# Optimization experiments

Measured on AMD Instinct MI355X. Metric: run time of the kernel, lower is better.

Reference implementation:

```python
import jax, jax.numpy as jnp
import numpy as np

D_MODEL = 1024
N_HEAD = 16
D_HEAD = D_MODEL // N_HEAD
FFN_HIDDEN = 4096
NEG_INF = -1e30


def sinusoid_pos_emb(pos_seq, d_model):
    # pos_seq: [K] descending relative positions; returns [K, d_model]
    inv_freq = 1.0 / (10000.0 ** (jnp.arange(0, d_model, 2, dtype=jnp.float32) / d_model))
    ang = pos_seq[:, None] * inv_freq[None, :]
    return jnp.concatenate([jnp.sin(ang), jnp.cos(ang)], axis=-1)


def rel_shift(x):
    # x: [B, H, Q, K] -> Transformer-XL relative shift
    b, h, q, k = x.shape
    x = jnp.pad(x, ((0, 0), (0, 0), (0, 0), (1, 0)))
    x = x.reshape(b, h, k + 1, q)[:, :, 1:, :].reshape(b, h, q, k)
    return x


def layer_norm(x, g, b, eps=1e-5):
    mu = jnp.mean(x, axis=-1, keepdims=True)
    var = jnp.var(x, axis=-1, keepdims=True)
    return (x - mu) * jax.lax.rsqrt(var + eps) * g + b


def setup_inputs() -> dict:
    key = jax.random.key(0)
    ks = jax.random.split(key, 20)
    B, T, M = 4, 2048, 2048
    s = 0.02
    inp = {
        "x": jax.random.normal(ks[0], (B, T, D_MODEL), jnp.float32),
        "mem": jax.random.normal(ks[1], (B, M, D_MODEL), jnp.float32),
        "Wq": jax.random.normal(ks[2], (D_MODEL, D_MODEL), jnp.float32) * s,
        "bq": jnp.zeros((D_MODEL,), jnp.float32),
        "Wk": jax.random.normal(ks[3], (D_MODEL, D_MODEL), jnp.float32) * s,
        "bk": jnp.zeros((D_MODEL,), jnp.float32),
        "Wv": jax.random.normal(ks[4], (D_MODEL, D_MODEL), jnp.float32) * s,
        "bv": jnp.zeros((D_MODEL,), jnp.float32),
        "Wo": jax.random.normal(ks[5], (D_MODEL, D_MODEL), jnp.float32) * s,
        "bo": jnp.zeros((D_MODEL,), jnp.float32),
        "Wr": jax.random.normal(ks[6], (D_MODEL, D_MODEL), jnp.float32) * s,
        "u": jax.random.normal(ks[7], (N_HEAD, D_HEAD), jnp.float32) * s,
        "v": jax.random.normal(ks[8], (N_HEAD, D_HEAD), jnp.float32) * s,
        "g1": jnp.ones((D_MODEL,), jnp.float32),
        "be1": jnp.zeros((D_MODEL,), jnp.float32),
        "g2": jnp.ones((D_MODEL,), jnp.float32),
        "be2": jnp.zeros((D_MODEL,), jnp.float32),
        "W1": jax.random.normal(ks[9], (D_MODEL, FFN_HIDDEN), jnp.float32) * s,
        "b1": jnp.zeros((FFN_HIDDEN,), jnp.float32),
        "W2": jax.random.normal(ks[10], (FFN_HIDDEN, D_MODEL), jnp.float32) * s,
        "b2": jnp.zeros((D_MODEL,), jnp.float32),
        "is_causal": 1,
    }
    return inp


def xl_attention(x, mem, Wq, bq, Wk, bk, Wv, bv, Wo, bo, Wr, u, v, is_causal):
    B, T, D = x.shape
    M = mem.shape[1]
    K = M + T
    c = jnp.concatenate([mem, x], axis=1)  # [B, K, D]
    q = (x @ Wq + bq).reshape(B, T, N_HEAD, D_HEAD)
    k = (c @ Wk + bk).reshape(B, K, N_HEAD, D_HEAD)
    vv = (c @ Wv + bv).reshape(B, K, N_HEAD, D_HEAD)
    pos_seq = jnp.arange(K - 1, -1, -1, dtype=jnp.float32)
    r = (sinusoid_pos_emb(pos_seq, D) @ Wr).reshape(K, N_HEAD, D_HEAD)
    # content term + relative-position term (Transformer-XL eq. A+C and B+D)
    AC = jnp.einsum('bihd,bjhd->bhij', q + u, k)
    BD = rel_shift(jnp.einsum('bihd,jhd->bhij', q + v, r))
    score = (AC + BD) * (1.0 / np.sqrt(D_HEAD))
    if is_causal:
        i = jnp.arange(T)[:, None]
        j = jnp.arange(K)[None, :]
        causal = (j <= i + M)  # query i may attend keys up to its own position
        score = jnp.where(causal[None, None], score, NEG_INF)
    attn = jax.nn.softmax(score, axis=-1)
    out = jnp.einsum('bhij,bjhd->bihd', attn, vv).reshape(B, T, D)
    return out @ Wo + bo


def reference(x, mem, Wq, bq, Wk, bk, Wv, bv, Wo, bo, Wr, u, v,
              g1, be1, g2, be2, W1, b1, W2, b2, is_causal):
    # dropout is identity at inference
    a = xl_attention(x, mem, Wq, bq, Wk, bk, Wv, bv, Wo, bo, Wr, u, v, is_causal)
    h = layer_norm(a + x, g1, be1)
    f = jax.nn.gelu(h @ W1 + b1) @ W2 + b2
    return layer_norm(f + h, g2, be2)
```

## Files before the change

### kernel.cpp

```cpp
#include <hip/hip_runtime.h>
#include <stdint.h>

typedef unsigned short u16;
typedef short s16x8 __attribute__((ext_vector_type(8)));
typedef unsigned short u16x4 __attribute__((ext_vector_type(4)));
typedef float f32x4 __attribute__((ext_vector_type(4)));

#define DEV static __device__ __forceinline__

DEV u16 f2b(float f) {
  union { float f; unsigned u; } v; v.f = f;
  unsigned r = v.u + 0x7fffu + ((v.u >> 16) & 1u);
  return (u16)(r >> 16);
}
DEV float b2f(u16 b) {
  union { unsigned u; float f; } v; v.u = ((unsigned)b) << 16; return v.f;
}
DEV unsigned pk_trunc(float a, float b) {
  return __builtin_amdgcn_perm(__float_as_uint(b), __float_as_uint(a), 0x07060302u);
}
DEV f32x4 MFMA16(s16x8 a, s16x8 b, f32x4 c) {
  return __builtin_amdgcn_mfma_f32_16x16x32_bf16(a, b, c, 0, 0, 0);
}
#define GLD_LDS16(gp, lp)                                                            \
  __builtin_amdgcn_global_load_lds((const __attribute__((address_space(1))) void*)(gp), \
                                   (__attribute__((address_space(3))) void*)(lp), 16, 0, 0)


__global__ __launch_bounds__(256) void wt_cast_t(const float* __restrict__ W,
                                                 u16* __restrict__ Wt, int Kd, int Nd) {
  __shared__ float tile[32][33];
  const int n0 = blockIdx.x * 32, k0 = blockIdx.y * 32;
  const int t = threadIdx.x;
#pragma unroll
  for (int p = 0; p < 4; ++p) {
    int idx = p * 256 + t; int r = idx >> 5, c = idx & 31;
    tile[r][c] = W[(long)(k0 + r) * Nd + n0 + c];
  }
  __syncthreads();
#pragma unroll
  for (int p = 0; p < 4; ++p) {
    int idx = p * 256 + t; int r = idx >> 5, c = idx & 31;
    Wt[(long)(n0 + r) * Kd + k0 + c] = f2b(tile[c][r]);
  }
}

__global__ __launch_bounds__(256) void build_cb(const float* __restrict__ x,
                                                const float* __restrict__ mem,
                                                u16* __restrict__ cb) {
  long idx = (long)blockIdx.x * 256 + threadIdx.x;
  long e4 = idx * 4;
  int b = (int)(e4 >> 22);
  long rem = e4 & ((1L << 22) - 1);
  int tok = (int)(rem >> 10);
  int d = (int)(rem & 1023);
  const float* src = (tok < 2048) ? &mem[((long)b * 2048 + tok) * 1024 + d]
                                  : &x[((long)b * 2048 + (tok - 2048)) * 1024 + d];
  float4 vv = *(const float4*)src;
  uint2 o;
  o.x = (unsigned)f2b(vv.x) | ((unsigned)f2b(vv.y) << 16);
  o.y = (unsigned)f2b(vv.z) | ((unsigned)f2b(vv.w) << 16);
  *(uint2*)&cb[e4] = o;
}

__global__ __launch_bounds__(256) void pos_emb(u16* __restrict__ pe) {
  const int d = blockIdx.x;
  const int e0 = threadIdx.x * 4;
  u16 o[4];
#pragma unroll
  for (int i = 0; i < 4; ++i) {
    int e = e0 + i;
    int f = (e < 512) ? e : (e - 512);
    float invf = expf(-(float)f * (9.210340371976184f / 512.f));
    float ang = (float)d * invf;
    o[i] = f2b((e < 512) ? sinf(ang) : cosf(ang));
  }
  uint2 pk; pk.x = (unsigned)o[0] | ((unsigned)o[1] << 16);
  pk.y = (unsigned)o[2] | ((unsigned)o[3] << 16);
  *(uint2*)&pe[(long)d * 1024 + e0] = pk;
}

#define EPI_BF16 0
#define EPI_F32 1
#define EPI_GELU 2
#define EPI_VT 3

template <int EPI, int QMAP>
__global__ __launch_bounds__(256) void gemm_bt(const u16* __restrict__ A,
                                               const u16* __restrict__ Bt,
                                               const float* __restrict__ bias,
                                               void* __restrict__ outp, int Ndim, int Kdim) {
  __shared__ __align__(16) u16 As[128 * 64];
  __shared__ __align__(16) u16 Bs[128 * 64];
  const int col0 = blockIdx.x * 128;
  const int row0 = blockIdx.y * 128;
  const int t = threadIdx.x;
  const int w = t >> 6, l = t & 63;
  const int wr = (w >> 1) * 64, wc = (w & 1) * 64;
  const int lr = l & 15, g = l >> 4;
  f32x4 acc[4][4];
#pragma unroll
  for (int m = 0; m < 4; ++m)
#pragma unroll
    for (int n = 0; n < 4; ++n) acc[m][n] = f32x4{0.f, 0.f, 0.f, 0.f};

  for (int k0 = 0; k0 < Kdim; k0 += 64) {
#pragma unroll
    for (int it = 0; it < 4; ++it) {
      int c = it * 256 + t;
      int r = c >> 3, ch = (c & 7) ^ (r & 7);
      long ga = row0 + r;
      if (QMAP) ga = ((ga >> 11) << 12) + 2048 + (ga & 2047);
      GLD_LDS16(A + ga * Kdim + k0 + ch * 8, &As[c * 8]);
      GLD_LDS16(Bt + (long)(col0 + r) * Kdim + k0 + ch * 8, &Bs[c * 8]);
    }
    __syncthreads();
#pragma unroll
    for (int kk = 0; kk < 2; ++kk) {
      s16x8 af[4], bfv[4];
#pragma unroll
      for (int m = 0; m < 4; ++m) {
        int rm = wr + m * 16 + lr;
        af[m] = *(const s16x8*)&As[rm * 64 + (((g + 4 * kk) ^ (rm & 7)) << 3)];
      }
#pragma unroll
      for (int n = 0; n < 4; ++n) {
        int rn = wc + n * 16 + lr;
        bfv[n] = *(const s16x8*)&Bs[rn * 64 + (((g + 4 * kk) ^ (rn & 7)) << 3)];
      }
#pragma unroll
      for (int m = 0; m < 4; ++m)
#pragma unroll
        for (int n = 0; n < 4; ++n) acc[m][n] = MFMA16(af[m], bfv[n], acc[m][n]);
    }
    __syncthreads();
  }

  const int lg = g * 4;
#pragma unroll
  for (int m = 0; m < 4; ++m) {
    int rbase = row0 + wr + m * 16 + lg;
#pragma unroll
    for (int n = 0; n < 4; ++n) {
      int gc = col0 + wc + n * 16 + lr;
      float bv = bias ? bias[gc] : 0.f;
#pragma unroll
      for (int rg = 0; rg < 4; ++rg) {
        float vv = acc[m][n][rg] + bv;
        ((u16*)outp)[(long)(rbase + rg) * Ndim + gc] = f2b(vv);
      }
    }
  }
}

template <int EPI, int QMAP, int BN>
__global__ __launch_bounds__(512) void gemm_big(const u16* __restrict__ A,
                                                const u16* __restrict__ Bt,
                                                const float* __restrict__ bias,
                                                void* __restrict__ outp, int Ndim, int Kdim) {
  constexpr int NF = BN / 64;
  __shared__ __align__(16) u16 As[2][256 * 64];
  __shared__ __align__(16) u16 Bs[2][BN * 64];
  const int col0 = blockIdx.x * BN;
  const int row0 = blockIdx.y * 256;
  const int t = threadIdx.x;
  const int w = t >> 6, l = t & 63;
  const int wr = (w >> 2) * 128, wc = (w & 3) * (BN / 4);
  const int lr = l & 15, g = l >> 4;

  f32x4 acc[8][NF];
#pragma unroll
  for (int m = 0; m < 8; ++m)
#pragma unroll
    for (int n = 0; n < NF; ++n) acc[m][n] = f32x4{0.f, 0.f, 0.f, 0.f};

  auto stageA = [&](int k0, int p, int nb) {
    int c = p * 512 + t;
    int r = c >> 3, ch = (c & 7) ^ (r & 7);
    long ga = row0 + r;
    if (QMAP) ga = ((ga >> 11) << 12) + 2048 + (ga & 2047);
    GLD_LDS16(A + ga * Kdim + k0 + ch * 8, &As[nb][c * 8]);
  };
  auto stageB = [&](int k0, int p, int nb) {
    int c = p * 512 + t;
    int r = c >> 3, ch = (c & 7) ^ (r & 7);
    GLD_LDS16(Bt + (long)(col0 + r) * Kdim + k0 + ch * 8, &Bs[nb][c * 8]);
  };

  const int nt = Kdim >> 6;
#pragma unroll
  for (int p = 0; p < 4; ++p) stageA(0, p, 0);
#pragma unroll
  for (int p = 0; p < NF; ++p) stageB(0, p, 0);
  __syncthreads();
  int cur = 0;

  for (int ti = 0; ti < nt; ++ti) {
    const int k1 = (ti + 1) << 6;
    const int nb = cur ^ 1;
    s16x8 bf[NF][2];
#pragma unroll
    for (int p = 0; p < 4; ++p) {
      s16x8 af[2][2];
#pragma unroll
      for (int i = 0; i < 2; ++i) {
        int rm = wr + (2 * p + i) * 16 + lr;
#pragma unroll
        for (int kk = 0; kk < 2; ++kk)
          af[i][kk] = *(const s16x8*)&As[cur][rm * 64 + (((g + 4 * kk) ^ (rm & 7)) << 3)];
      }
      if (p == 0) {
#pragma unroll
        for (int n = 0; n < NF; ++n) {
          int rn = wc + n * 16 + lr;
#pragma unroll
          for (int kk = 0; kk < 2; ++kk)
            bf[n][kk] = *(const s16x8*)&Bs[cur][rn * 64 + (((g + 4 * kk) ^ (rn & 7)) << 3)];
        }
      }
      if (ti + 1 < nt) {
        if (p == 0) { stageA(k1, 0, nb); stageB(k1, 0, nb); }
        else if (p == 1) { stageA(k1, 1, nb); if (NF > 1) stageB(k1, 1, nb); }
        else if (p == 2) {
          stageA(k1, 2, nb); stageA(k1, 3, nb);
          if (NF == 4) { stageB(k1, 2, nb); stageB(k1, 3, nb); }
        }
      }
      __builtin_amdgcn_s_barrier();
      __builtin_amdgcn_s_setprio(1);
#pragma unroll
      for (int i = 0; i < 2; ++i)
#pragma unroll
        for (int n = 0; n < NF; ++n) {
          acc[2 * p + i][n] = MFMA16(af[i][0], bf[n][0], acc[2 * p + i][n]);
          acc[2 * p + i][n] = MFMA16(af[i][1], bf[n][1], acc[2 * p + i][n]);
        }
      __builtin_amdgcn_s_setprio(0);
      if (p < 3) __builtin_amdgcn_s_barrier();
    }
    __syncthreads();
    cur ^= 1;
  }

  const int lg = g * 4;
#pragma unroll
  for (int m = 0; m < 8; ++m) {
    int rbase = row0 + wr + m * 16 + lg;
#pragma unroll
    for (int n = 0; n < NF; ++n) {
      int gc = col0 + wc + n * 16 + lr;
      float bv = bias ? bias[gc] : 0.f;
#pragma unroll
      for (int rg = 0; rg < 4; ++rg) {
        int grow = rbase + rg;
        float vv = acc[m][n][rg] + bv;
        if (EPI == EPI_GELU) {
          float x3 = vv * vv * vv;
          vv = 0.5f * vv * (1.f + tanhf(0.7978845608028654f * (vv + 0.044715f * x3)));
        }
        if (EPI == EPI_F32) {
          ((float*)outp)[(long)grow * Ndim + gc] = vv;
        } else if (EPI == EPI_VT) {
          int bb = grow >> 12, tok = grow & 4095;
          int hh = gc >> 6, dd = gc & 63;
          ((u16*)outp)[((long)((bb * 16 + hh) * 64 + dd) << 12) + tok] = f2b(vv);
        } else {
          ((u16*)outp)[(long)grow * Ndim + gc] = f2b(vv);
        }
      }
    }
  }
}

#define SCALE_LOG2 0.18033688011111793f

__global__ __launch_bounds__(1024, 4) void attn_fused(
    const u16* __restrict__ qg, const u16* __restrict__ kg, const u16* __restrict__ vTg,
    const u16* __restrict__ rg, const float* __restrict__ u, const float* __restrict__ vparam,
    const int* __restrict__ causal_p, u16* __restrict__ Og) {
  __shared__ __align__(16) u16 Ks[2][64 * 64];
  __shared__ __align__(16) u16 Vs[2][64 * 64];
  __shared__ __align__(16) u16 GPs[16][16 * 84];

  const int bh = blockIdx.x, b = bh >> 4, h = bh & 15;
  const int i0 = (int)(gridDim.y - 1 - blockIdx.y) * 256;
  const int t = threadIdx.x, w = t >> 6, l = t & 63;
  const int q = l & 15, g = l >> 4, lk = g * 8;
  const int causal = causal_p[0];

  const long kbase = ((long)b * 4096) * 1024 + h * 64;
  const long vbase = ((long)((b * 16 + h) * 64)) * 4096;

  const int irow = i0 + 16 * w + q;
  const u16* qp = qg + ((long)(b * 2048 + irow)) * 1024 + h * 64;
  s16x8 qlo = *(const s16x8*)(qp + lk);
  s16x8 qhi = *(const s16x8*)(qp + 32 + lk);
  s16x8 qu0, qu1, qv0, qv1;
#pragma unroll
  for (int j = 0; j < 8; ++j) {
    float a0 = b2f((u16)qlo[j]), a1 = b2f((u16)qhi[j]);
    float uu0 = u[h * 64 + lk + j], vv0 = vparam[h * 64 + lk + j];
    float uu1 = u[h * 64 + 32 + lk + j], vv1 = vparam[h * 64 + 32 + lk + j];
    qu0[j] = (short)f2b((a0 + uu0) * SCALE_LOG2); qv0[j] = (short)f2b((a0 + vv0) * SCALE_LOG2);
    qu1[j] = (short)f2b((a1 + uu1) * SCALE_LOG2); qv1[j] = (short)f2b((a1 + vv1) * SCALE_LOG2);
  }

  float lsum = 0.f;
  f32x4 oacc[4];
#pragma unroll
  for (int n = 0; n < 4; ++n) oacc[n] = f32x4{0.f, 0.f, 0.f, 0.f};

  u16* gpw = &GPs[w][0];
  const int kc0 = q * 64 + ((g ^ (q & 7)) << 3);
  const int kc1 = kc0 ^ 32;
  const int gq = q * 85 + 63;
  const int gst = q * 84 + 4 * g;
  const int pst = q * 72 + 4 * g;
  const int prd = q * 72 + lk;

  auto STAGE = [&](int j0s, int bufi) {
    int t9 = t & 511;
    int rrow = t9 >> 3, gch = (t9 & 7) ^ (rrow & 7);
    if (t < 512) GLD_LDS16(kg + kbase + (long)(j0s + rrow) * 1024 + gch * 8, &Ks[bufi][t9 * 8]);
    else         GLD_LDS16(vTg + vbase + (long)rrow * 4096 + j0s + gch * 8, &Vs[bufi][t9 * 8]);
  };

  s16x8 rf0[5], rf1[5];
  auto LOADR = [&](int j0r) {
    const int dlo = 2048 + i0 + 16 * w - j0r - 63;
#pragma unroll
    for (int tt = 0; tt < 5; ++tt) {
      int d = dlo + tt * 16 + q; d = min(max(d, 0), 4095);
      const u16* rp = rg + ((long)d << 10) + h * 64;
      rf0[tt] = *(const s16x8*)(rp + lk);
      rf1[tt] = *(const s16x8*)(rp + 32 + lk);
    }
  };

  const int jmax = causal ? (2048 + i0 + 256) : 4096;
  const int nt = jmax >> 6;
  const int jlimit = 2048 + i0 + 16 * w + 15;

  STAGE(0, 0);
  LOADR(0);
  int cur = 0;

  for (int ti = 0; ti < nt; ++ti) {
    const int j0 = ti << 6;
    __syncthreads();
    if (ti + 1 < nt) STAGE((ti + 1) << 6, cur ^ 1);

    if (!causal || j0 <= jlimit) {
      const u16* ksp = &Ks[cur][0];
      const u16* vsp = &Vs[cur][0];

      f32x4 sv[4];
      __builtin_amdgcn_s_setprio(1);
#pragma unroll
      for (int n = 0; n < 4; ++n) {
        s16x8 af0 = *(const s16x8*)&ksp[kc0 + n * 1024];
        s16x8 af1 = *(const s16x8*)&ksp[kc1 + n * 1024];
        f32x4 z = f32x4{0.f, 0.f, 0.f, 0.f};
        z = MFMA16(af0, qu0, z);
        z = MFMA16(af1, qu1, z);
        sv[n] = z;
      }
#pragma unroll
      for (int tt = 0; tt < 5; ++tt) {
        f32x4 z = f32x4{0.f, 0.f, 0.f, 0.f};
        z = MFMA16(rf0[tt], qv0, z);
        z = MFMA16(rf1[tt], qv1, z);
        uint2 gp2 = {pk_trunc(z[0], z[1]), pk_trunc(z[2], z[3])};
        *(u16x4*)&gpw[gst + tt * 16] = __builtin_bit_cast(u16x4, gp2);
      }
      __builtin_amdgcn_s_setprio(0);

      if (ti + 1 < nt && (!causal || j0 + 64 <= jlimit)) LOADR(j0 + 64);

      const bool need_mask = (causal != 0) && (j0 + 63 > 2048 + i0 + 16 * w);
#pragma unroll
      for (int n = 0; n < 4; ++n) {
#pragma unroll
        for (int r = 0; r < 4; ++r) {
          int j = 16 * n + 4 * g + r;
          float bd = b2f(gpw[gq - j]);
          float scv = sv[n][r] + bd;
          if (need_mask && (j0 + j > 2048 + irow)) scv = -3.0e38f;
          sv[n][r] = scv;
        }
      }
      float ls = 0.f;
#pragma unroll
      for (int n = 0; n < 4; ++n) {
        float p0 = __builtin_amdgcn_exp2f(sv[n][0]);
        float p1 = __builtin_amdgcn_exp2f(sv[n][1]);
        float p2 = __builtin_amdgcn_exp2f(sv[n][2]);
        float p3 = __builtin_amdgcn_exp2f(sv[n][3]);
        ls += (p0 + p1) + (p2 + p3);
        uint2 pp = {pk_trunc(p0, p1), pk_trunc(p2, p3)};
        *(u16x4*)&gpw[pst + n * 16] = __builtin_bit_cast(u16x4, pp);
      }
      lsum += ls;

      s16x8 pb0 = *(const s16x8*)&gpw[prd];
      s16x8 pb1 = *(const s16x8*)&gpw[prd + 32];
      __builtin_amdgcn_s_setprio(1);
#pragma unroll
      for (int n = 0; n < 4; ++n) {
        s16x8 va0 = *(const s16x8*)&vsp[kc0 + n * 1024];
        s16x8 va1 = *(const s16x8*)&vsp[kc1 + n * 1024];
        oacc[n] = MFMA16(va0, pb0, oacc[n]);
        oacc[n] = MFMA16(va1, pb1, oacc[n]);
      }
      __builtin_amdgcn_s_setprio(0);
    }
    cur ^= 1;
  }

  lsum += __shfl_xor(lsum, 16);
  lsum += __shfl_xor(lsum, 32);
  const float linv = 1.f / lsum;
  const long obase = (long)(b * 2048 + irow) * 1024 + h * 64;
#pragma unroll
  for (int n = 0; n < 4; ++n) {
    u16x4 ov = {f2b(oacc[n][0] * linv), f2b(oacc[n][1] * linv),
                f2b(oacc[n][2] * linv), f2b(oacc[n][3] * linv)};
    *(u16x4*)&Og[obase + n * 16 + 4 * g] = ov;
  }
}

template <int WRITE_BF16>
__global__ __launch_bounds__(256) void ln_res(const float* __restrict__ a,
                                              const float* __restrict__ resid,
                                              const float* __restrict__ g,
                                              const float* __restrict__ be,
                                              float* __restrict__ outf, u16* __restrict__ outb) {
  const int row = blockIdx.x;
  const int t = threadIdx.x;
  const long base = (long)row * 1024;
  float4 av = *(const float4*)&a[base + t * 4];
  float4 rv = *(const float4*)&resid[base + t * 4];
  float x0 = av.x + rv.x, x1 = av.y + rv.y, x2 = av.z + rv.z, x3 = av.w + rv.w;
  float s = x0 + x1 + x2 + x3;
  float q = x0 * x0 + x1 * x1 + x2 * x2 + x3 * x3;
#pragma unroll
  for (int d = 1; d < 64; d <<= 1) {
    s += __shfl_xor(s, d);
    q += __shfl_xor(q, d);
  }
  __shared__ float ss[4], sq[4];
  if ((t & 63) == 0) { ss[t >> 6] = s; sq[t >> 6] = q; }
  __syncthreads();
  s = ss[0] + ss[1] + ss[2] + ss[3];
  q = sq[0] + sq[1] + sq[2] + sq[3];
  float mu = s * (1.f / 1024.f);
  float var = q * (1.f / 1024.f) - mu * mu;
  float rstd = rsqrtf(var + 1e-5f);
  float4 gv = *(const float4*)&g[t * 4];
  float4 bv = *(const float4*)&be[t * 4];
  float y0 = (x0 - mu) * rstd * gv.x + bv.x;
  float y1 = (x1 - mu) * rstd * gv.y + bv.y;
  float y2 = (x2 - mu) * rstd * gv.z + bv.z;
  float y3 = (x3 - mu) * rstd * gv.w + bv.w;
  float4 ov = {y0, y1, y2, y3};
  *(float4*)&outf[base + t * 4] = ov;
  if (WRITE_BF16) {
    uint2 o;
    o.x = (unsigned)f2b(y0) | ((unsigned)f2b(y1) << 16);
    o.y = (unsigned)f2b(y2) | ((unsigned)f2b(y3) << 16);
    *(uint2*)&outb[base + t * 4] = o;
  }
}

extern "C" void kernel_launch(void* const* d_in, const int* in_sizes, int n_in, void* d_out,
                              int out_size, void* d_ws, size_t ws_size, hipStream_t stream) {
  const float* x = (const float*)d_in[0];
  const float* mem = (const float*)d_in[1];
  const float* Wq = (const float*)d_in[2];
  const float* bq = (const float*)d_in[3];
  const float* Wk = (const float*)d_in[4];
  const float* bk = (const float*)d_in[5];
  const float* Wv = (const float*)d_in[6];
  const float* bv = (const float*)d_in[7];
  const float* Wo = (const float*)d_in[8];
  const float* bo = (const float*)d_in[9];
  const float* Wr = (const float*)d_in[10];
  const float* u = (const float*)d_in[11];
  const float* vp = (const float*)d_in[12];
  const float* g1 = (const float*)d_in[13];
  const float* be1 = (const float*)d_in[14];
  const float* g2 = (const float*)d_in[15];
  const float* be2 = (const float*)d_in[16];
  const float* W1 = (const float*)d_in[17];
  const float* b1 = (const float*)d_in[18];
  const float* W2 = (const float*)d_in[19];
  const float* b2 = (const float*)d_in[20];
  const int* iscaus = (const int*)d_in[21];

  char* ws = (char*)d_ws;
  const size_t MB = 1024 * 1024;
  u16* WqT = (u16*)(ws + 0 * MB);
  u16* WkT = (u16*)(ws + 2 * MB);
  u16* WvT = (u16*)(ws + 4 * MB);
  u16* WoT = (u16*)(ws + 6 * MB);
  u16* WrT = (u16*)(ws + 8 * MB);
  u16* W1T = (u16*)(ws + 10 * MB);
  u16* W2T = (u16*)(ws + 18 * MB);
  u16* cb = (u16*)(ws + 26 * MB);
  float* proj = (float*)(ws + 26 * MB);
  u16* pe = (u16*)(ws + 58 * MB);
  u16* qb = (u16*)(ws + 66 * MB);
  u16* kb = (u16*)(ws + 82 * MB);
  u16* vT = (u16*)(ws + 114 * MB);
  u16* rb = (u16*)(ws + 146 * MB);
  u16* aO = (u16*)(ws + 154 * MB);
  u16* hb = (u16*)(ws + 154 * MB);
  u16* f1 = (u16*)(ws + 58 * MB);
  float* f2 = (float*)(ws + 122 * MB);
  (void)ws_size; (void)in_sizes; (void)n_in; (void)out_size;

  wt_cast_t<<<dim3(32, 32), 256, 0, stream>>>(Wq, WqT, 1024, 1024);
  wt_cast_t<<<dim3(32, 32), 256, 0, stream>>>(Wk, WkT, 1024, 1024);
  wt_cast_t<<<dim3(32, 32), 256, 0, stream>>>(Wv, WvT, 1024, 1024);
  wt_cast_t<<<dim3(32, 32), 256, 0, stream>>>(Wo, WoT, 1024, 1024);
  wt_cast_t<<<dim3(32, 32), 256, 0, stream>>>(Wr, WrT, 1024, 1024);
  wt_cast_t<<<dim3(128, 32), 256, 0, stream>>>(W1, W1T, 1024, 4096);
  wt_cast_t<<<dim3(32, 128), 256, 0, stream>>>(W2, W2T, 4096, 1024);

  build_cb<<<16384, 256, 0, stream>>>(x, mem, cb);
  pos_emb<<<4096, 256, 0, stream>>>(pe);

  gemm_big<EPI_BF16, 1, 128><<<dim3(8, 32), 512, 0, stream>>>(cb, WqT, bq, qb, 1024, 1024);
  gemm_big<EPI_BF16, 0, 256><<<dim3(4, 64), 512, 0, stream>>>(cb, WkT, bk, kb, 1024, 1024);
  gemm_big<EPI_VT, 0, 256><<<dim3(4, 64), 512, 0, stream>>>(cb, WvT, bv, vT, 1024, 1024);
  gemm_bt<EPI_BF16, 0><<<dim3(8, 32), 256, 0, stream>>>(pe, WrT, nullptr, rb, 1024, 1024);

  attn_fused<<<dim3(64, 8), 1024, 0, stream>>>(qb, kb, vT, rb, u, vp, iscaus, aO);

  gemm_big<EPI_F32, 0, 128><<<dim3(8, 32), 512, 0, stream>>>(aO, WoT, bo, proj, 1024, 1024);
  ln_res<1><<<8192, 256, 0, stream>>>(proj, x, g1, be1, proj, hb);

  gemm_big<EPI_GELU, 0, 256><<<dim3(16, 32), 512, 0, stream>>>(hb, W1T, b1, f1, 4096, 1024);
  gemm_big<EPI_F32, 0, 128><<<dim3(8, 32), 512, 0, stream>>>(f1, W2T, b2, f2, 1024, 4096);
  ln_res<0><<<8192, 256, 0, stream>>>(f2, proj, g2, be2, (float*)d_out, nullptr);
}
```

Baseline: 911.7 us.

## Triple-buffer gemm_big with vmcnt waits and fix tile width at 128

```diff
diff --git a/kernel.cpp b/kernel.cpp
--- a/kernel.cpp
+++ b/kernel.cpp
@@ -153,93 +153,77 @@
   }
 }
 
-template <int EPI, int QMAP, int BN>
+template <int EPI, int QMAP>
 __global__ __launch_bounds__(512) void gemm_big(const u16* __restrict__ A,
                                                 const u16* __restrict__ Bt,
                                                 const float* __restrict__ bias,
                                                 void* __restrict__ outp, int Ndim, int Kdim) {
-  constexpr int NF = BN / 64;
-  __shared__ __align__(16) u16 As[2][256 * 64];
-  __shared__ __align__(16) u16 Bs[2][BN * 64];
-  const int col0 = blockIdx.x * BN;
+  __shared__ __align__(16) u16 As[3][256 * 64];
+  __shared__ __align__(16) u16 Bs[3][128 * 64];
+  const int col0 = blockIdx.x * 128;
   const int row0 = blockIdx.y * 256;
   const int t = threadIdx.x;
   const int w = t >> 6, l = t & 63;
-  const int wr = (w >> 2) * 128, wc = (w & 3) * (BN / 4);
+  const int wr = (w >> 2) * 128, wc = (w & 3) * 32;
   const int lr = l & 15, g = l >> 4;
 
-  f32x4 acc[8][NF];
-#pragma unroll
-  for (int m = 0; m < 8; ++m)
-#pragma unroll
-    for (int n = 0; n < NF; ++n) acc[m][n] = f32x4{0.f, 0.f, 0.f, 0.f};
-
-  auto stageA = [&](int k0, int p, int nb) {
-    int c = p * 512 + t;
-    int r = c >> 3, ch = (c & 7) ^ (r & 7);
-    long ga = row0 + r;
-    if (QMAP) ga = ((ga >> 11) << 12) + 2048 + (ga & 2047);
-    GLD_LDS16(A + ga * Kdim + k0 + ch * 8, &As[nb][c * 8]);
+  f32x4 acc[8][2];
+#pragma unroll
+  for (int m = 0; m < 8; ++m) {
+    acc[m][0] = f32x4{0.f, 0.f, 0.f, 0.f};
+    acc[m][1] = f32x4{0.f, 0.f, 0.f, 0.f};
+  }
+
+  auto STG = [&](int k0, int nb) {
+#pragma unroll
+    for (int p = 0; p < 4; ++p) {
+      int c = p * 512 + t;
+      int r = c >> 3, ch = (c & 7) ^ (r & 7);
+      long ga = row0 + r;
+      if (QMAP) ga = ((ga >> 11) << 12) + 2048 + (ga & 2047);
+      GLD_LDS16(A + ga * Kdim + k0 + ch * 8, &As[nb][c * 8]);
+    }
+#pragma unroll
+    for (int p = 0; p < 2; ++p) {
+      int c = p * 512 + t;
+      int r = c >> 3, ch = (c & 7) ^ (r & 7);
+      GLD_LDS16(Bt + (long)(col0 + r) * Kdim + k0 + ch * 8, &Bs[nb][c * 8]);
+    }
   };
-  auto stageB = [&](int k0, int p, int nb) {
-    int c = p * 512 + t;
-    int r = c >> 3, ch = (c & 7) ^ (r & 7);
-    GLD_LDS16(Bt + (long)(col0 + r) * Kdim + k0 + ch * 8, &Bs[nb][c * 8]);
-  };
 
   const int nt = Kdim >> 6;
-#pragma unroll
-  for (int p = 0; p < 4; ++p) stageA(0, p, 0);
-#pragma unroll
-  for (int p = 0; p < NF; ++p) stageB(0, p, 0);
-  __syncthreads();
+  STG(0, 0);
+  if (nt > 1) STG(64, 1);
   int cur = 0;
 
   for (int ti = 0; ti < nt; ++ti) {
-    const int k1 = (ti + 1) << 6;
-    const int nb = cur ^ 1;
-    s16x8 bf[NF][2];
-#pragma unroll
-    for (int p = 0; p < 4; ++p) {
-      s16x8 af[2][2];
-#pragma unroll
-      for (int i = 0; i < 2; ++i) {
-        int rm = wr + (2 * p + i) * 16 + lr;
-#pragma unroll
-        for (int kk = 0; kk < 2; ++kk)
-          af[i][kk] = *(const s16x8*)&As[cur][rm * 64 + (((g + 4 * kk) ^ (rm & 7)) << 3)];
-      }
-      if (p == 0) {
-#pragma unroll
-        for (int n = 0; n < NF; ++n) {
-          int rn = wc + n * 16 + lr;
-#pragma unroll
-          for (int kk = 0; kk < 2; ++kk)
-            bf[n][kk] = *(const s16x8*)&Bs[cur][rn * 64 + (((g + 4 * kk) ^ (rn & 7)) << 3)];
-        }
-      }
-      if (ti + 1 < nt) {
-        if (p == 0) { stageA(k1, 0, nb); stageB(k1, 0, nb); }
-        else if (p == 1) { stageA(k1, 1, nb); if (NF > 1) stageB(k1, 1, nb); }
-        else if (p == 2) {
-          stageA(k1, 2, nb); stageA(k1, 3, nb);
-          if (NF == 4) { stageB(k1, 2, nb); stageB(k1, 3, nb); }
-        }
-      }
-      __builtin_amdgcn_s_barrier();
-      __builtin_amdgcn_s_setprio(1);
-#pragma unroll
-      for (int i = 0; i < 2; ++i)
-#pragma unroll
-        for (int n = 0; n < NF; ++n) {
-          acc[2 * p + i][n] = MFMA16(af[i][0], bf[n][0], acc[2 * p + i][n]);
-          acc[2 * p + i][n] = MFMA16(af[i][1], bf[n][1], acc[2 * p + i][n]);
-        }
-      __builtin_amdgcn_s_setprio(0);
-      if (p < 3) __builtin_amdgcn_s_barrier();
-    }
-    __syncthreads();
-    cur ^= 1;
+    if (ti + 1 < nt) asm volatile("s_waitcnt vmcnt(6)\n\ts_barrier" ::: "memory");
+    else             asm volatile("s_waitcnt vmcnt(0)\n\ts_barrier" ::: "memory");
+    if (ti + 2 < nt) STG((ti + 2) << 6, (ti + 2) % 3);
+
+    const u16* as = &As[cur][0];
+    const u16* bs = &Bs[cur][0];
+    s16x8 bf[2][2];
+#pragma unroll
+    for (int n = 0; n < 2; ++n) {
+      int rn = wc + n * 16 + lr;
+#pragma unroll
+      for (int kk = 0; kk < 2; ++kk)
+        bf[n][kk] = *(const s16x8*)&bs[rn * 64 + (((g + 4 * kk) ^ (rn & 7)) << 3)];
+    }
+    __builtin_amdgcn_s_setprio(1);
+#pragma unroll
+    for (int m = 0; m < 8; ++m) {
+      int rm = wr + m * 16 + lr;
+      s16x8 a0 = *(const s16x8*)&as[rm * 64 + ((g ^ (rm & 7)) << 3)];
+      s16x8 a1 = *(const s16x8*)&as[rm * 64 + (((g + 4) ^ (rm & 7)) << 3)];
+      acc[m][0] = MFMA16(a0, bf[0][0], acc[m][0]);
+      acc[m][0] = MFMA16(a1, bf[0][1], acc[m][0]);
+      acc[m][1] = MFMA16(a0, bf[1][0], acc[m][1]);
+      acc[m][1] = MFMA16(a1, bf[1][1], acc[m][1]);
+    }
+    __builtin_amdgcn_s_setprio(0);
+    cur = (cur == 2) ? 0 : cur + 1;
   }
 
   const int lg = g * 4;
@@ -247,7 +231,7 @@
   for (int m = 0; m < 8; ++m) {
     int rbase = row0 + wr + m * 16 + lg;
 #pragma unroll
-    for (int n = 0; n < NF; ++n) {
+    for (int n = 0; n < 2; ++n) {
       int gc = col0 + wc + n * 16 + lr;
       float bv = bias ? bias[gc] : 0.f;
 #pragma unroll
@@ -530,17 +514,17 @@
   build_cb<<<16384, 256, 0, stream>>>(x, mem, cb);
   pos_emb<<<4096, 256, 0, stream>>>(pe);
 
-  gemm_big<EPI_BF16, 1, 128><<<dim3(8, 32), 512, 0, stream>>>(cb, WqT, bq, qb, 1024, 1024);
-  gemm_big<EPI_BF16, 0, 256><<<dim3(4, 64), 512, 0, stream>>>(cb, WkT, bk, kb, 1024, 1024);
-  gemm_big<EPI_VT, 0, 256><<<dim3(4, 64), 512, 0, stream>>>(cb, WvT, bv, vT, 1024, 1024);
+  gemm_big<EPI_BF16, 1><<<dim3(8, 32), 512, 0, stream>>>(cb, WqT, bq, qb, 1024, 1024);
+  gemm_big<EPI_BF16, 0><<<dim3(8, 64), 512, 0, stream>>>(cb, WkT, bk, kb, 1024, 1024);
+  gemm_big<EPI_VT, 0><<<dim3(8, 64), 512, 0, stream>>>(cb, WvT, bv, vT, 1024, 1024);
   gemm_bt<EPI_BF16, 0><<<dim3(8, 32), 256, 0, stream>>>(pe, WrT, nullptr, rb, 1024, 1024);
 
   attn_fused<<<dim3(64, 8), 1024, 0, stream>>>(qb, kb, vT, rb, u, vp, iscaus, aO);
 
-  gemm_big<EPI_F32, 0, 128><<<dim3(8, 32), 512, 0, stream>>>(aO, WoT, bo, proj, 1024, 1024);
+  gemm_big<EPI_F32, 0><<<dim3(8, 32), 512, 0, stream>>>(aO, WoT, bo, proj, 1024, 1024);
   ln_res<1><<<8192, 256, 0, stream>>>(proj, x, g1, be1, proj, hb);
 
-  gemm_big<EPI_GELU, 0, 256><<<dim3(16, 32), 512, 0, stream>>>(hb, W1T, b1, f1, 4096, 1024);
-  gemm_big<EPI_F32, 0, 128><<<dim3(8, 32), 512, 0, stream>>>(f1, W2T, b2, f2, 1024, 4096);
+  gemm_big<EPI_GELU, 0><<<dim3(32, 32), 512, 0, stream>>>(hb, W1T, b1, f1, 4096, 1024);
+  gemm_big<EPI_F32, 0><<<dim3(8, 32), 512, 0, stream>>>(f1, W2T, b2, f2, 1024, 4096);
   ln_res<0><<<8192, 256, 0, stream>>>(f2, proj, g2, be2, (float*)d_out, nullptr);
 }
```

New measurement: 980.4 us. +7.5%, slower.
